# Performance work log

Hardware: AMD Instinct MI355X
Metric: run time of the kernel (lower is better)

The kernel has to match this reference:

```python
import jax, jax.numpy as jnp
import numpy as np

H, DH, BS = 12, 64, 64          # heads, head_dim, block_size
D, FF, L, EPS = 768, 3072, 12, 1e-12

def _ln(x, g, b):
    m = x.mean(-1, keepdims=True)
    v = ((x - m) ** 2).mean(-1, keepdims=True)
    return (x - m) * jax.lax.rsqrt(v + EPS) * g + b

def setup_inputs() -> dict:
    key = jax.random.key(0)
    ks = iter(jax.random.split(key, 40))
    B, S, IN, C = 2, 4096, 1280, 2
    nb = S // BS
    def p(shape, s=0.02):
        return jax.random.normal(next(ks), shape, jnp.float32) * s
    inp = dict(
        embeddings=jax.random.normal(next(ks), (B, S, IN), jnp.float32),
        attention_mask=jnp.ones((B, S), jnp.int32),
        Wp=p((IN, D)), bp=jnp.zeros((D,), jnp.float32),
        pos_emb=p((S, D)), tok_emb=p((D,)),
        lne_g=jnp.ones((D,), jnp.float32), lne_b=jnp.zeros((D,), jnp.float32),
        Wq=p((L, D, D)), bq=jnp.zeros((L, D), jnp.float32),
        Wk=p((L, D, D)), bk=jnp.zeros((L, D), jnp.float32),
        Wv=p((L, D, D)), bv=jnp.zeros((L, D), jnp.float32),
        Wo=p((L, D, D)), bo=jnp.zeros((L, D), jnp.float32),
        l1g=jnp.ones((L, D), jnp.float32), l1b=jnp.zeros((L, D), jnp.float32),
        W1=p((L, D, FF)), b1=jnp.zeros((L, FF), jnp.float32),
        W2=p((L, FF, D)), b2=jnp.zeros((L, D), jnp.float32),
        l2g=jnp.ones((L, D), jnp.float32), l2b=jnp.zeros((L, D), jnp.float32),
        Wc=p((D, C)), bc=jnp.zeros((C,), jnp.float32),
    )
    # BigBird pattern: each interior query block -> 2 global + 3 window + 3 random key blocks.
    # Random blocks are drawn once (deterministic) like HF's data-independent rand mask.
    rng = np.random.default_rng(0)
    idx, val = [], []
    for i in range(1, nb - 1):
        blocks = [0, nb - 1, i - 1, i, i + 1]
        v = [True, True, i - 1 != 0, True, i + 1 != nb - 1]  # dedupe window/global overlap
        forbid = set(blocks)
        allowed = [x for x in range(nb) if x not in forbid]
        r = rng.choice(allowed, size=3, replace=False).tolist()
        idx.append(blocks + r)
        val.append(v + [True, True, True])
    inp["blk_idx"] = jnp.asarray(np.array(idx, np.int32))    # [nb-2, 8]
    inp["blk_valid"] = jnp.asarray(np.array(val, bool))       # [nb-2, 8]
    return inp

def reference(embeddings, attention_mask, Wp, bp, pos_emb, tok_emb, lne_g, lne_b,
              Wq, bq, Wk, bk, Wv, bv, Wo, bo, l1g, l1b, W1, b1, W2, b2, l2g, l2b,
              Wc, bc, blk_idx, blk_valid):
    B, S, _ = embeddings.shape
    nb = S // BS
    na = blk_idx.shape[1]
    x = embeddings @ Wp + bp + pos_emb + tok_emb
    x = _ln(x, lne_g, lne_b)
    am = attention_mask.astype(jnp.float32)                       # [B,S]
    full_bias = ((am - 1.0) * 1e9)[:, None, None, None, :]        # [B,1,1,1,S]
    amb = am.reshape(B, nb, BS)
    am_g = amb[:, blk_idx].reshape(B, nb - 2, na * BS)            # gathered key mask
    vmask = jnp.repeat(blk_valid, BS, axis=-1)                    # [nb-2, na*BS]
    gb = jnp.where((am_g > 0) & vmask[None], 0.0, -1e9)[:, None, :, None, :]
    scale = 1.0 / np.sqrt(DH).astype(np.float32)

    def layer(x, p):
        wq, bq_, wk, bk_, wv, bv_, wo, bo_, g1, b1_, w1, bi1, w2, bi2, g2, b2_ = p
        q = (x @ wq + bq_).reshape(B, S, H, DH).transpose(0, 2, 1, 3)
        k = (x @ wk + bk_).reshape(B, S, H, DH).transpose(0, 2, 1, 3)
        v = (x @ wv + bv_).reshape(B, S, H, DH).transpose(0, 2, 1, 3)
        qb = q.reshape(B, H, nb, BS, DH)
        kb = k.reshape(B, H, nb, BS, DH)
        vb = v.reshape(B, H, nb, BS, DH)
        # interior query blocks: gather sparse key blocks (global+window+random)
        q_int = qb[:, :, 1:-1]                                     # [B,H,nb-2,BS,DH]
        k_g = kb[:, :, blk_idx].reshape(B, H, nb - 2, na * BS, DH)
        v_g = vb[:, :, blk_idx].reshape(B, H, nb - 2, na * BS, DH)
        s = jnp.einsum('bhiqd,bhikd->bhiqk', q_int, k_g) * scale + gb
        p_ = jax.nn.softmax(s, axis=-1)
        ctx_int = jnp.einsum('bhiqk,bhikd->bhiqd', p_, v_g)
        # first/last blocks are global: attend to all keys
        q_edge = jnp.stack([qb[:, :, 0], qb[:, :, -1]], axis=2)    # [B,H,2,BS,DH]
        se = jnp.einsum('bheqd,bhkd->bheqk', q_edge, k) * scale + full_bias
        pe = jax.nn.softmax(se, axis=-1)
        ctx_e = jnp.einsum('bheqk,bhkd->bheqd', pe, v)
        ctx = jnp.concatenate([ctx_e[:, :, :1], ctx_int, ctx_e[:, :, 1:]], axis=2)
        ctx = ctx.reshape(B, H, S, DH).transpose(0, 2, 1, 3).reshape(B, S, D)
        x = _ln(x + ctx @ wo + bo_, g1, b1_)
        h = jax.nn.gelu(x @ w1 + bi1, approximate=False) @ w2 + bi2
        x = _ln(x + h, g2, b2_)
        return x, None

    x, _ = jax.lax.scan(layer, x, (Wq, bq, Wk, bk, Wv, bv, Wo, bo,
                                   l1g, l1b, W1, b1, W2, b2, l2g, l2b))
    return x[:, 0, :] @ Wc + bc
```

## Files before the change

### kernel.cpp

```cpp
#include <hip/hip_runtime.h>
#include <hip/hip_bf16.h>
#include <math.h>

using bf16 = __hip_bfloat16;
typedef short bf16x8 __attribute__((ext_vector_type(8)));
typedef float f32x4 __attribute__((ext_vector_type(4)));
typedef unsigned short u16x4 __attribute__((ext_vector_type(4)));
typedef unsigned short u16x8 __attribute__((ext_vector_type(8)));
typedef short bf16x4v __attribute__((ext_vector_type(4)));

#define DEV __device__ __forceinline__

constexpr int BATCH = 2, SEQ = 4096, INPD = 1280, DM = 768, FFD = 3072;
constexpr int NL = 12, NH = 12, DHD = 64, NBLK = 64, NCLS = 2;
constexpr int MR = BATCH * SEQ;
constexpr int QKVN = 3 * DM;
constexpr int NJOBS = 62 + 16;
constexpr int PARTF = 64 * 64 + 128;

DEV void gload_lds16(const void* g, void* l) {
  __builtin_amdgcn_global_load_lds(
      (const __attribute__((address_space(1))) unsigned int*)g,
      (__attribute__((address_space(3))) unsigned int*)l, 16, 0, 0);
}

DEV f32x4 mfma16(bf16x8 a, bf16x8 b, f32x4 c) {
  return __builtin_amdgcn_mfma_f32_16x16x32_bf16(a, b, c, 0, 0, 0);
}

DEV float b2f(unsigned short u) { return __uint_as_float((unsigned)u << 16); }
DEV unsigned short f2b(float x) {
  bf16 h = __float2bfloat16(x);
  return *(unsigned short*)&h;
}

DEV int xcd_swizzle(int orig, int nwg) {
  int q = nwg >> 3, r = nwg & 7;
  int xcd = orig & 7, pos_ = orig >> 3;
  return (xcd < r ? xcd * (q + 1) : r * (q + 1) + (xcd - r) * q) + pos_;
}

__global__ void k_f32_to_bf16(const float* __restrict__ in, bf16* __restrict__ out, int n) {
  int i = (blockIdx.x * blockDim.x + threadIdx.x) * 8;
  int stride = gridDim.x * blockDim.x * 8;
  for (; i < n; i += stride) {
    float4 a = *(const float4*)(in + i);
    float4 b = *(const float4*)(in + i + 4);
    bf16 t8[8];
    t8[0] = __float2bfloat16(a.x); t8[1] = __float2bfloat16(a.y);
    t8[2] = __float2bfloat16(a.z); t8[3] = __float2bfloat16(a.w);
    t8[4] = __float2bfloat16(b.x); t8[5] = __float2bfloat16(b.y);
    t8[6] = __float2bfloat16(b.z); t8[7] = __float2bfloat16(b.w);
    *(bf16x8*)(out + i) = *(bf16x8*)t8;
  }
}

DEV void tr32_tile(const float* __restrict__ src, bf16* __restrict__ dst,
                   int K, int N, int tile, float t[32][33], int tid) {
  int nt = N >> 5;
  int tk = tile / nt, tn = tile - tk * nt;
  {
    int k = tid >> 3, c4 = (tid & 7) << 2;
    float4 v = *(const float4*)(src + (size_t)(tk * 32 + k) * N + tn * 32 + c4);
    t[k][c4 + 0] = v.x; t[k][c4 + 1] = v.y; t[k][c4 + 2] = v.z; t[k][c4 + 3] = v.w;
  }
  __syncthreads();
  {
    int n = tid >> 3, kc = (tid & 7) << 2;
    bf16 o4[4];
    o4[0] = __float2bfloat16(t[kc + 0][n]);
    o4[1] = __float2bfloat16(t[kc + 1][n]);
    o4[2] = __float2bfloat16(t[kc + 2][n]);
    o4[3] = __float2bfloat16(t[kc + 3][n]);
    *(bf16x4v*)(dst + (size_t)(tn * 32 + n) * K + tk * 32 + kc) = *(bf16x4v*)o4;
  }
}

__global__ __launch_bounds__(256) void k_transpose_one(const float* __restrict__ src,
                                                       bf16* __restrict__ dst, int K, int N) {
  __shared__ float t[32][33];
  tr32_tile(src, dst, K, N, blockIdx.x, t, threadIdx.x);
}

__global__ __launch_bounds__(256) void k_transpose_layer(
    const float* __restrict__ Wq, const float* __restrict__ Wk,
    const float* __restrict__ Wv, const float* __restrict__ Wo,
    const float* __restrict__ W1, const float* __restrict__ W2,
    bf16* __restrict__ wqkvT, bf16* __restrict__ woT,
    bf16* __restrict__ w1T, bf16* __restrict__ w2T, int l) {
  __shared__ float t[32][33];
  int id = blockIdx.x;
  const float* src; bf16* dst; int K, N;
  if (id < 1728) {
    int m = id / 576; id -= m * 576;
    src = (m == 0 ? Wq : m == 1 ? Wk : Wv) + (size_t)l * DM * DM;
    dst = wqkvT + (size_t)m * DM * DM; K = DM; N = DM;
  } else if (id < 2304) {
    id -= 1728; src = Wo + (size_t)l * DM * DM; dst = woT; K = DM; N = DM;
  } else if (id < 4608) {
    id -= 2304; src = W1 + (size_t)l * DM * FFD; dst = w1T; K = DM; N = FFD;
  } else {
    id -= 4608; src = W2 + (size_t)l * FFD * DM; dst = w2T; K = FFD; N = DM;
  }
  tr32_tile(src, dst, K, N, id, t, threadIdx.x);
}

template <int EPI>
__global__ __launch_bounds__(256) void k_gemm(
    const bf16* __restrict__ A, const bf16* __restrict__ BT, int N, int K,
    const float* __restrict__ b0, const float* __restrict__ pos, const float* __restrict__ tok,
    bf16* __restrict__ Cb) {
  __shared__ __align__(16) bf16 lA[2][128 * 32];
  __shared__ __align__(16) bf16 lB[2][128 * 32];
  const int tid = threadIdx.x;
  const int gx = gridDim.x;
  const int tile = xcd_swizzle(blockIdx.y * gx + blockIdx.x, gx * gridDim.y);
  const int bx = tile % gx, by = tile / gx;
  const int bm = by * 128, bn = bx * 128;
  const int lane = tid & 63, wid = tid >> 6;
  const int wm = (wid >> 1) * 64, wn = (wid & 1) * 64;
  const int lr = lane & 15, lks = lane >> 4;
  const bf16* Abase = A + (size_t)bm * K;
  const bf16* Bbase = BT + (size_t)bn * K;

  auto stage = [&](int buf, int t) {
    int k0 = t << 5;
#pragma unroll
    for (int ss = 0; ss < 2; ++ss) {
      int seg = tid + ss * 256;
      int row = seg >> 2, slot = seg & 3;
      int kseg = slot ^ ((row >> 1) & 3);
      gload_lds16(Abase + (size_t)row * K + k0 + kseg * 8, &lA[buf][seg * 8]);
      gload_lds16(Bbase + (size_t)row * K + k0 + kseg * 8, &lB[buf][seg * 8]);
    }
  };

  f32x4 acc[4][4] = {};
  const int nt = K >> 5;
  stage(0, 0);
  __syncthreads();
  for (int t = 0; t < nt; ++t) {
    const int buf = t & 1;
    if (t + 1 < nt) stage(buf ^ 1, t + 1);
    bf16x8 af[4], bfr[4];
#pragma unroll
    for (int m = 0; m < 4; ++m) {
      int rr = wm + m * 16 + lr;
      af[m] = *(const bf16x8*)(&lA[buf][rr * 32 + ((lks ^ ((rr >> 1) & 3)) << 3)]);
    }
#pragma unroll
    for (int n = 0; n < 4; ++n) {
      int rr = wn + n * 16 + lr;
      bfr[n] = *(const bf16x8*)(&lB[buf][rr * 32 + ((lks ^ ((rr >> 1) & 3)) << 3)]);
    }
#pragma unroll
    for (int m = 0; m < 4; ++m)
#pragma unroll
      for (int n = 0; n < 4; ++n)
        acc[m][n] = mfma16(af[m], bfr[n], acc[m][n]);
    __syncthreads();
  }
  const int gq = lane >> 4;
#pragma unroll
  for (int m = 0; m < 4; ++m) {
#pragma unroll
    for (int n = 0; n < 4; ++n) {
      int gcol = bn + wn + n * 16 + lr;
      f32x4 v = acc[m][n];
#pragma unroll
      for (int rr = 0; rr < 4; ++rr) {
        int grow = bm + wm + m * 16 + gq * 4 + rr;
        float x = v[rr];
        if constexpr (EPI == 2) {
          x += b0[gcol];
        } else {
          x += b0[gcol] + pos[(size_t)(grow & (SEQ - 1)) * N + gcol] + tok[gcol];
        }
        Cb[(size_t)grow * N + gcol] = __float2bfloat16(x);
      }
    }
  }
}

template <int EPI>
__global__ __launch_bounds__(512) void k_gemm_big(
    const bf16* __restrict__ A, const bf16* __restrict__ BT, int N, int K,
    const float* __restrict__ b0, const float* __restrict__ b1, const float* __restrict__ b2,
    bf16* __restrict__ Cb) {
  __shared__ __align__(16) bf16 lA[2][256 * 32];
  __shared__ __align__(16) bf16 lB[2][128 * 32];
  const int tid = threadIdx.x;
  const int gx = gridDim.x;
  const int tile = xcd_swizzle(blockIdx.y * gx + blockIdx.x, gx * gridDim.y);
  const int bx = tile % gx, by = tile / gx;
  const int bm = by * 256, bn = bx * 128;
  const int lane = tid & 63, wid = tid >> 6;
  const int wm = (wid >> 1) * 64, wn = (wid & 1) * 64;
  const int lr = lane & 15, lks = lane >> 4;
  const bf16* Abase = A + (size_t)bm * K;
  const bf16* Bbase = BT + (size_t)bn * K;

  auto stage = [&](int buf, int t) {
    int k0 = t << 5;
#pragma unroll
    for (int ss = 0; ss < 2; ++ss) {
      int seg = tid + ss * 512;
      int row = seg >> 2, slot = seg & 3;
      int kseg = slot ^ ((row >> 1) & 3);
      gload_lds16(Abase + (size_t)row * K + k0 + kseg * 8, &lA[buf][seg * 8]);
    }
    {
      int row = tid >> 2, slot = tid & 3;
      int kseg = slot ^ ((row >> 1) & 3);
      gload_lds16(Bbase + (size_t)row * K + k0 + kseg * 8, &lB[buf][tid * 8]);
    }
  };

  f32x4 acc[4][4] = {};
  const int nt = K >> 5;
  stage(0, 0);
  __syncthreads();
  for (int t = 0; t < nt; ++t) {
    const int buf = t & 1;
    if (t + 1 < nt) stage(buf ^ 1, t + 1);
    bf16x8 af[4], bfr[4];
#pragma unroll
    for (int m = 0; m < 4; ++m) {
      int rr = wm + m * 16 + lr;
      af[m] = *(const bf16x8*)(&lA[buf][rr * 32 + ((lks ^ ((rr >> 1) & 3)) << 3)]);
    }
#pragma unroll
    for (int n = 0; n < 4; ++n) {
      int rr = wn + n * 16 + lr;
      bfr[n] = *(const bf16x8*)(&lB[buf][rr * 32 + ((lks ^ ((rr >> 1) & 3)) << 3)]);
    }
#pragma unroll
    for (int m = 0; m < 4; ++m)
#pragma unroll
      for (int n = 0; n < 4; ++n)
        acc[m][n] = mfma16(af[m], bfr[n], acc[m][n]);
    __syncthreads();
  }
  const int gq = lane >> 4;
#pragma unroll
  for (int m = 0; m < 4; ++m) {
#pragma unroll
    for (int n = 0; n < 4; ++n) {
      int gcol = bn + wn + n * 16 + lr;
      f32x4 v = acc[m][n];
#pragma unroll
      for (int rr = 0; rr < 4; ++rr) {
        int grow = bm + wm + m * 16 + gq * 4 + rr;
        float x = v[rr];
        if constexpr (EPI == 0) {
          int c = gcol; const float* bb = b0;
          if (c >= 2 * DM) { bb = b2; c -= 2 * DM; }
          else if (c >= DM) { bb = b1; c -= DM; }
          x += bb[c];
        } else {
          x += b0[gcol];
          x = 0.5f * x * (1.0f + erff(x * 0.70710678118654752f));
        }
        Cb[(size_t)grow * N + gcol] = __float2bfloat16(x);
      }
    }
  }
}

template <bool HASRES>
__global__ __launch_bounds__(256) void k_ln_res(
    const bf16* __restrict__ gout, const bf16* res,
    const float* __restrict__ g, const float* __restrict__ b,
    bf16* out) {
  const int wv = threadIdx.x >> 6, lane = threadIdx.x & 63;
  const int row = blockIdx.x * 4 + wv;
  const unsigned short* gp = (const unsigned short*)gout + (size_t)row * DM;
  const unsigned short* rp = (const unsigned short*)res + (size_t)row * DM;
  float v[12];
  float s = 0.f, s2 = 0.f;
#pragma unroll
  for (int i = 0; i < 3; ++i) {
    const int c = i * 256 + lane * 4;
    u16x4 a4 = *(const u16x4*)(gp + c);
    u16x4 r4;
    if constexpr (HASRES) r4 = *(const u16x4*)(rp + c);
#pragma unroll
    for (int k2 = 0; k2 < 4; ++k2) {
      float x = b2f(a4[k2]);
      if constexpr (HASRES) x += b2f(r4[k2]);
      v[i * 4 + k2] = x;
      s += x; s2 += x * x;
    }
  }
#pragma unroll
  for (int off = 1; off < 64; off <<= 1) {
    s += __shfl_xor(s, off);
    s2 += __shfl_xor(s2, off);
  }
  const float mean = s * (1.0f / DM);
  const float var = s2 * (1.0f / DM) - mean * mean;
  const float rs = rsqrtf(var + 1e-12f);
  unsigned short* op = (unsigned short*)out + (size_t)row * DM;
#pragma unroll
  for (int i = 0; i < 3; ++i) {
    const int c = i * 256 + lane * 4;
    float4 g4 = *(const float4*)(g + c);
    float4 b4 = *(const float4*)(b + c);
    u16x4 o4;
    o4[0] = f2b((v[i * 4 + 0] - mean) * rs * g4.x + b4.x);
    o4[1] = f2b((v[i * 4 + 1] - mean) * rs * g4.y + b4.y);
    o4[2] = f2b((v[i * 4 + 2] - mean) * rs * g4.z + b4.z);
    o4[3] = f2b((v[i * 4 + 3] - mean) * rs * g4.w + b4.w);
    *(u16x4*)(op + c) = o4;
  }
}

__global__ __launch_bounds__(256) void k_vt(const bf16* __restrict__ qkv, bf16* __restrict__ vt) {
  __shared__ unsigned short t[64][72];
  const int bh = blockIdx.y, t0 = blockIdx.x * 64;
  const int b = bh / NH, h = bh - b * NH;
  const int tid = threadIdx.x;
  const int rr = tid >> 2, cs = (tid & 3) * 16;
  const unsigned short* src = (const unsigned short*)qkv +
      (size_t)(b * SEQ + t0 + rr) * QKVN + 2 * DM + h * DHD + cs;
  u16x8 v0 = *(const u16x8*)(src);
  u16x8 v1 = *(const u16x8*)(src + 8);
#pragma unroll
  for (int i = 0; i < 8; ++i) { t[cs + i][rr] = v0[i]; t[cs + 8 + i][rr] = v1[i]; }
  __syncthreads();
  unsigned short* dst = (unsigned short*)vt + (size_t)(bh * DHD + rr) * SEQ + t0 + cs;
  u16x8 o0, o1;
#pragma unroll
  for (int i = 0; i < 8; ++i) { o0[i] = t[rr][cs + i]; o1[i] = t[rr][cs + 8 + i]; }
  *(u16x8*)(dst) = o0;
  *(u16x8*)(dst + 8) = o1;
}

__global__ __launch_bounds__(256) void k_attn(
    const bf16* __restrict__ qkv, const bf16* __restrict__ vt,
    const int* __restrict__ blk_idx,
    bf16* __restrict__ ctx, float* __restrict__ epart) {
  __shared__ __align__(16) bf16 sQ[64 * 64];
  __shared__ __align__(16) bf16 sK[2][64 * 64];
  __shared__ __align__(16) bf16 sV[2][64 * 64];
  __shared__ __align__(16) bf16 sP[4][16 * 64];
  const int job = blockIdx.x;
  const int b = job / (NH * NJOBS);
  const int rem = job - b * NH * NJOBS;
  const int h = rem / NJOBS;
  const int j = rem - h * NJOBS;
  const int tid = threadIdx.x, lane = tid & 63, w = tid >> 6;
  const int lr = lane & 15, lks = lane >> 4;

  const bool interior = (j < 62);
  int qblk, e = 0, split = 0;
  if (interior) qblk = j + 1;
  else { int tt = j - 62; e = tt >> 3; split = tt & 7; qblk = e ? NBLK - 1 : 0; }
  const int qt0 = qblk * 64;

  const int skip_pos = interior ? (j == 0 ? 2 : (j == 61 ? 4 : 8)) : 8;
  const int nkb = (skip_pos < 8) ? 7 : 8;
  auto kbi_of = [&](int i) {
    int kb = i + (i >= skip_pos ? 1 : 0);
    return interior ? blk_idx[j * 8 + kb] : split * 8 + kb;
  };

  const bf16* kbase0 = qkv + (size_t)b * SEQ * QKVN + DM + h * DHD;
  const bf16* vbase0 = vt + (size_t)((b * NH + h) * DHD) * SEQ;
  auto stageKV = [&](int buf, int kbi) {
    const int kt0 = kbi * 64;
#pragma unroll
    for (int ss = 0; ss < 2; ++ss) {
      int seg = tid + ss * 256;
      int row = seg >> 3, slot = seg & 7;
      int kseg = slot ^ (row & 7);
      gload_lds16(kbase0 + (size_t)(kt0 + row) * QKVN + kseg * 8, &sK[buf][seg * 8]);
      gload_lds16(vbase0 + (size_t)row * SEQ + kt0 + kseg * 8, &sV[buf][seg * 8]);
    }
  };

  {
    const bf16* qbase = qkv + (size_t)(b * SEQ + qt0) * QKVN + h * DHD;
#pragma unroll
    for (int ss = 0; ss < 2; ++ss) {
      int seg = tid + ss * 256;
      int row = seg >> 3, slot = seg & 7;
      int kseg = slot ^ (row & 7);
      gload_lds16(qbase + (size_t)row * QKVN + kseg * 8, sQ + seg * 8);
    }
  }
  stageKV(0, kbi_of(0));
  __syncthreads();
  bf16x8 aq[2];
#pragma unroll
  for (int kk = 0; kk < 2; ++kk) {
    int rq = w * 16 + lr;
    int slot = (kk * 4 + lks) ^ (rq & 7);
    aq[kk] = *(const bf16x8*)(sQ + rq * 64 + slot * 8);
  }

  float m_r[4], l_r[4];
  f32x4 o[4] = {};
#pragma unroll
  for (int r = 0; r < 4; ++r) { m_r[r] = -1e30f; l_r[r] = 0.f; }

  for (int i = 0; i < nkb; ++i) {
    const int buf = i & 1;
    if (i + 1 < nkb) stageKV(buf ^ 1, kbi_of(i + 1));
    f32x4 sfr[4];
#pragma unroll
    for (int n = 0; n < 4; ++n) {
      f32x4 z = {};
#pragma unroll
      for (int kk = 0; kk < 2; ++kk) {
        int rk = n * 16 + lr;
        int slot = (kk * 4 + lks) ^ (rk & 7);
        bf16x8 kf = *(const bf16x8*)(&sK[buf][rk * 64 + slot * 8]);
        z = mfma16(aq[kk], kf, z);
      }
      sfr[n] = z;
    }
#pragma unroll
    for (int n = 0; n < 4; ++n)
#pragma unroll
      for (int r = 0; r < 4; ++r) sfr[n][r] *= 0.125f;
    float alpha[4];
#pragma unroll
    for (int r = 0; r < 4; ++r) {
      float tmx = fmaxf(fmaxf(sfr[0][r], sfr[1][r]), fmaxf(sfr[2][r], sfr[3][r]));
#pragma unroll
      for (int off = 1; off < 16; off <<= 1) tmx = fmaxf(tmx, __shfl_xor(tmx, off));
      float mnew = fmaxf(m_r[r], tmx);
      alpha[r] = __expf(m_r[r] - mnew);
      m_r[r] = mnew;
    }
#pragma unroll
    for (int r = 0; r < 4; ++r) {
      float su = 0.f;
#pragma unroll
      for (int n = 0; n < 4; ++n) {
        float p = __expf(sfr[n][r] - m_r[r]);
        sfr[n][r] = p;
        su += p;
      }
#pragma unroll
      for (int off = 1; off < 16; off <<= 1) su += __shfl_xor(su, off);
      l_r[r] = l_r[r] * alpha[r] + su;
    }
#pragma unroll
    for (int n = 0; n < 4; ++n) {
#pragma unroll
      for (int r = 0; r < 4; ++r) {
        int prow = lks * 4 + r;
        int col = n * 16 + lr;
        int eo = prow * 64 + ((((col >> 3) ^ (prow & 7)) << 3) | (col & 7));
        sP[w][eo] = __float2bfloat16(sfr[n][r]);
      }
    }
#pragma unroll
    for (int n = 0; n < 4; ++n)
#pragma unroll
      for (int r = 0; r < 4; ++r) o[n][r] *= alpha[r];
    asm volatile("s_waitcnt lgkmcnt(0)" ::: "memory");
    __builtin_amdgcn_sched_barrier(0);
    bf16x8 pa[2];
#pragma unroll
    for (int kk = 0; kk < 2; ++kk) {
      int slot = (kk * 4 + lks) ^ (lr & 7);
      pa[kk] = *(const bf16x8*)(sP[w] + lr * 64 + slot * 8);
    }
#pragma unroll
    for (int n = 0; n < 4; ++n) {
#pragma unroll
      for (int kk = 0; kk < 2; ++kk) {
        int rv = n * 16 + lr;
        int slot = (kk * 4 + lks) ^ (rv & 7);
        bf16x8 vf = *(const bf16x8*)(&sV[buf][rv * 64 + slot * 8]);
        o[n] = mfma16(pa[kk], vf, o[n]);
      }
    }
    __syncthreads();
  }
  if (interior) {
#pragma unroll
    for (int r = 0; r < 4; ++r) {
      float inv = 1.0f / l_r[r];
      int tok = qt0 + w * 16 + lks * 4 + r;
#pragma unroll
      for (int n = 0; n < 4; ++n) {
        int col = h * DHD + n * 16 + lr;
        ctx[(size_t)(b * SEQ + tok) * DM + col] = __float2bfloat16(o[n][r] * inv);
      }
    }
  } else {
    float* base = epart + (size_t)((((b * NH + h) * 2 + e) * 8) + split) * PARTF;
#pragma unroll
    for (int r = 0; r < 4; ++r) {
      int qrow = w * 16 + lks * 4 + r;
#pragma unroll
      for (int n = 0; n < 4; ++n)
        base[qrow * 64 + n * 16 + lr] = o[n][r];
      if (lr == 0) { base[4096 + qrow] = m_r[r]; base[4096 + 64 + qrow] = l_r[r]; }
    }
  }
}

__global__ __launch_bounds__(256) void k_combine(const float* __restrict__ epart,
                                                 bf16* __restrict__ ctx) {
  const int bid = blockIdx.x;
  const int b = bid / (NH * 2);
  const int rem = bid - b * NH * 2;
  const int h = rem >> 1, e = rem & 1;
  const int tid = threadIdx.x;
  const int row = tid >> 2, cq = tid & 3;
  const float* base0 = epart + (size_t)(((b * NH + h) * 2 + e) * 8) * PARTF;
  float ms[8], ls[8], M = -1e30f;
#pragma unroll
  for (int s = 0; s < 8; ++s) {
    const float* bp = base0 + (size_t)s * PARTF;
    ms[s] = bp[4096 + row];
    ls[s] = bp[4096 + 64 + row];
    M = fmaxf(M, ms[s]);
  }
  float Lt = 0.f, accv[16];
#pragma unroll
  for (int i = 0; i < 16; ++i) accv[i] = 0.f;
#pragma unroll
  for (int s = 0; s < 8; ++s) {
    float wgt = __expf(ms[s] - M);
    Lt += ls[s] * wgt;
    const float* op = base0 + (size_t)s * PARTF + row * 64 + cq * 16;
#pragma unroll
    for (int i = 0; i < 16; ++i) accv[i] += op[i] * wgt;
  }
  float inv = 1.0f / Lt;
  int qblk = e ? NBLK - 1 : 0;
  int tok = qblk * 64 + row;
  bf16* cp = ctx + (size_t)(b * SEQ + tok) * DM + h * DHD + cq * 16;
#pragma unroll
  for (int i = 0; i < 16; ++i) cp[i] = __float2bfloat16(accv[i] * inv);
}

__global__ void k_classifier(const bf16* __restrict__ xb, const float* __restrict__ Wc,
                             const float* __restrict__ bc, float* __restrict__ out) {
  const int tid = threadIdx.x, lane = tid & 63, wv = tid >> 6;
  const int b = wv >> 1, c = wv & 1;
  float s = 0.f;
  for (int d = lane; d < DM; d += 64)
    s += __bfloat162float(xb[(size_t)(b * SEQ) * DM + d]) * Wc[d * NCLS + c];
#pragma unroll
  for (int off = 32; off > 0; off >>= 1) s += __shfl_down(s, off);
  if (lane == 0) out[b * NCLS + c] = s + bc[c];
}

extern "C" void kernel_launch(void* const* d_in, const int* in_sizes, int n_in,
                              void* d_out, int out_size, void* d_ws, size_t ws_size,
                              hipStream_t stream) {
  const float* embeddings = (const float*)d_in[0];
  const float* Wp  = (const float*)d_in[2];
  const float* bp  = (const float*)d_in[3];
  const float* pos = (const float*)d_in[4];
  const float* tokv = (const float*)d_in[5];
  const float* lng = (const float*)d_in[6];
  const float* lnb = (const float*)d_in[7];
  const float* Wq  = (const float*)d_in[8];
  const float* bq  = (const float*)d_in[9];
  const float* Wk  = (const float*)d_in[10];
  const float* bk  = (const float*)d_in[11];
  const float* Wv  = (const float*)d_in[12];
  const float* bv  = (const float*)d_in[13];
  const float* Wo  = (const float*)d_in[14];
  const float* bo  = (const float*)d_in[15];
  const float* l1g = (const float*)d_in[16];
  const float* l1b = (const float*)d_in[17];
  const float* W1  = (const float*)d_in[18];
  const float* b1  = (const float*)d_in[19];
  const float* W2  = (const float*)d_in[20];
  const float* b2  = (const float*)d_in[21];
  const float* l2g = (const float*)d_in[22];
  const float* l2b = (const float*)d_in[23];
  const float* Wc  = (const float*)d_in[24];
  const float* bc  = (const float*)d_in[25];
  const int*  bidx = (const int*)d_in[26];
  (void)in_sizes; (void)n_in; (void)out_size; (void)ws_size;

  char* ws = (char*)d_ws;
  size_t off = 0;
  auto alloc = [&](size_t bytes) -> char* {
    char* p = ws + off;
    off += (bytes + 255) & ~(size_t)255;
    return p;
  };
  bf16*  embB  = (bf16*)alloc((size_t)MR * INPD * 2);
  bf16*  wpT   = (bf16*)alloc((size_t)DM * INPD * 2);
  bf16*  wqkvT = (bf16*)alloc((size_t)QKVN * DM * 2);
  bf16*  woT   = (bf16*)alloc((size_t)DM * DM * 2);
  bf16*  w1T   = (bf16*)alloc((size_t)FFD * DM * 2);
  bf16*  w2T   = (bf16*)alloc((size_t)DM * FFD * 2);
  bf16*  xb    = (bf16*)alloc((size_t)MR * DM * 2);
  bf16*  gout  = (bf16*)alloc((size_t)MR * DM * 2);
  bf16*  qkvB  = (bf16*)alloc((size_t)MR * QKVN * 2);
  bf16*  vtB   = (bf16*)alloc((size_t)BATCH * NH * DHD * SEQ * 2);
  bf16*  ctxB  = (bf16*)alloc((size_t)MR * DM * 2);
  bf16*  hB    = (bf16*)alloc((size_t)MR * FFD * 2);
  float* epart = (float*)alloc((size_t)BATCH * NH * 2 * 8 * PARTF * 4);

  k_f32_to_bf16<<<2048, 256, 0, stream>>>(embeddings, embB, MR * INPD);
  k_transpose_one<<<(INPD / 32) * (DM / 32), 256, 0, stream>>>(Wp, wpT, INPD, DM);
  k_gemm<3><<<dim3(DM / 128, MR / 128), 256, 0, stream>>>(embB, wpT, DM, INPD,
      bp, pos, tokv, gout);
  k_ln_res<false><<<MR / 4, 256, 0, stream>>>(gout, gout, lng, lnb, xb);

  for (int l = 0; l < NL; ++l) {
    k_transpose_layer<<<6912, 256, 0, stream>>>(Wq, Wk, Wv, Wo, W1, W2,
        wqkvT, woT, w1T, w2T, l);
    k_gemm_big<0><<<dim3(QKVN / 128, MR / 256), 512, 0, stream>>>(xb, wqkvT, QKVN, DM,
        bq + (size_t)l * DM, bk + (size_t)l * DM, bv + (size_t)l * DM, qkvB);
    k_vt<<<dim3(SEQ / 64, BATCH * NH), 256, 0, stream>>>(qkvB, vtB);
    k_attn<<<BATCH * NH * NJOBS, 256, 0, stream>>>(qkvB, vtB, bidx, ctxB, epart);
    k_combine<<<BATCH * NH * 2, 256, 0, stream>>>(epart, ctxB);
    k_gemm<2><<<dim3(DM / 128, MR / 128), 256, 0, stream>>>(ctxB, woT, DM, DM,
        bo + (size_t)l * DM, nullptr, nullptr, gout);
    k_ln_res<true><<<MR / 4, 256, 0, stream>>>(gout, xb,
        l1g + (size_t)l * DM, l1b + (size_t)l * DM, xb);
    k_gemm_big<1><<<dim3(FFD / 128, MR / 256), 512, 0, stream>>>(xb, w1T, FFD, DM,
        b1 + (size_t)l * FFD, nullptr, nullptr, hB);
    k_gemm<2><<<dim3(DM / 128, MR / 128), 256, 0, stream>>>(hB, w2T, DM, FFD,
        b2 + (size_t)l * DM, nullptr, nullptr, gout);
    k_ln_res<true><<<MR / 4, 256, 0, stream>>>(gout, xb,
        l2g + (size_t)l * DM, l2b + (size_t)l * DM, xb);
  }
  k_classifier<<<1, 256, 0, stream>>>(xb, Wc, bc, (float*)d_out);
}
```

Baseline: 3.504 ms.

## Prune last layer to CLS rows and fuse V transpose into QKV GEMM

The output reads only token 0 of each batch, so the final layer now computes attention for the first global query block only. Its output projection, LayerNorms and FFN run as GEMVs on two rows. Separately, the QKV GEMM epilogue writes V straight into the transposed layout, which removes the k_vt kernel and its extra pass over memory. The pruning is a legitimate dead-code elimination, but the last layer's K/V are still computed in full, and the transposed V write is a strided 8-byte scatter.

```diff
diff --git a/kernel.cpp b/kernel.cpp
--- a/kernel.cpp
+++ b/kernel.cpp
@@ -186,7 +186,7 @@
 __global__ __launch_bounds__(512) void k_gemm_big(
     const bf16* __restrict__ A, const bf16* __restrict__ BT, int N, int K,
     const float* __restrict__ b0, const float* __restrict__ b1, const float* __restrict__ b2,
-    bf16* __restrict__ Cb) {
+    bf16* __restrict__ vt, bf16* __restrict__ Cb) {
   __shared__ __align__(16) bf16 lA[2][256 * 32];
   __shared__ __align__(16) bf16 lB[2][128 * 32];
   const int tid = threadIdx.x;
@@ -247,21 +247,33 @@
 #pragma unroll
     for (int n = 0; n < 4; ++n) {
       int gcol = bn + wn + n * 16 + lr;
+      int grow0 = bm + wm + m * 16 + gq * 4;
       f32x4 v = acc[m][n];
-#pragma unroll
-      for (int rr = 0; rr < 4; ++rr) {
-        int grow = bm + wm + m * 16 + gq * 4 + rr;
-        float x = v[rr];
-        if constexpr (EPI == 0) {
-          int c = gcol; const float* bb = b0;
-          if (c >= 2 * DM) { bb = b2; c -= 2 * DM; }
-          else if (c >= DM) { bb = b1; c -= DM; }
-          x += bb[c];
+      if constexpr (EPI == 0) {
+        if (gcol < 2 * DM) {
+          const float* bb = (gcol < DM) ? b0 : b1;
+          float bias = bb[(gcol < DM) ? gcol : gcol - DM];
+#pragma unroll
+          for (int rr = 0; rr < 4; ++rr)
+            Cb[(size_t)(grow0 + rr) * N + gcol] = __float2bfloat16(v[rr] + bias);
         } else {
-          x += b0[gcol];
+          int c = gcol - 2 * DM;
+          float bias = b2[c];
+          int h = c >> 6, d = c & 63;
+          int bq_ = grow0 >> 12, s = grow0 & (SEQ - 1);
+          bf16 o4[4];
+#pragma unroll
+          for (int rr = 0; rr < 4; ++rr) o4[rr] = __float2bfloat16(v[rr] + bias);
+          *(bf16x4v*)(vt + ((size_t)((bq_ * NH + h) * DHD + d)) * SEQ + s) = *(bf16x4v*)o4;
+        }
+      } else {
+        float bias = b0[gcol];
+#pragma unroll
+        for (int rr = 0; rr < 4; ++rr) {
+          float x = v[rr] + bias;
           x = 0.5f * x * (1.0f + erff(x * 0.70710678118654752f));
+          Cb[(size_t)(grow0 + rr) * N + gcol] = __float2bfloat16(x);
         }
-        Cb[(size_t)grow * N + gcol] = __float2bfloat16(x);
       }
     }
   }
@@ -315,40 +327,19 @@
   }
 }
 
-__global__ __launch_bounds__(256) void k_vt(const bf16* __restrict__ qkv, bf16* __restrict__ vt) {
-  __shared__ unsigned short t[64][72];
-  const int bh = blockIdx.y, t0 = blockIdx.x * 64;
-  const int b = bh / NH, h = bh - b * NH;
-  const int tid = threadIdx.x;
-  const int rr = tid >> 2, cs = (tid & 3) * 16;
-  const unsigned short* src = (const unsigned short*)qkv +
-      (size_t)(b * SEQ + t0 + rr) * QKVN + 2 * DM + h * DHD + cs;
-  u16x8 v0 = *(const u16x8*)(src);
-  u16x8 v1 = *(const u16x8*)(src + 8);
-#pragma unroll
-  for (int i = 0; i < 8; ++i) { t[cs + i][rr] = v0[i]; t[cs + 8 + i][rr] = v1[i]; }
-  __syncthreads();
-  unsigned short* dst = (unsigned short*)vt + (size_t)(bh * DHD + rr) * SEQ + t0 + cs;
-  u16x8 o0, o1;
-#pragma unroll
-  for (int i = 0; i < 8; ++i) { o0[i] = t[rr][cs + i]; o1[i] = t[rr][cs + 8 + i]; }
-  *(u16x8*)(dst) = o0;
-  *(u16x8*)(dst + 8) = o1;
-}
-
 __global__ __launch_bounds__(256) void k_attn(
     const bf16* __restrict__ qkv, const bf16* __restrict__ vt,
     const int* __restrict__ blk_idx,
-    bf16* __restrict__ ctx, float* __restrict__ epart) {
+    bf16* __restrict__ ctx, float* __restrict__ epart, int nj, int jbase) {
   __shared__ __align__(16) bf16 sQ[64 * 64];
   __shared__ __align__(16) bf16 sK[2][64 * 64];
   __shared__ __align__(16) bf16 sV[2][64 * 64];
   __shared__ __align__(16) bf16 sP[4][16 * 64];
   const int job = blockIdx.x;
-  const int b = job / (NH * NJOBS);
-  const int rem = job - b * NH * NJOBS;
-  const int h = rem / NJOBS;
-  const int j = rem - h * NJOBS;
+  const int b = job / (NH * nj);
+  const int rem = job - b * NH * nj;
+  const int h = rem / nj;
+  const int j = jbase + (rem - h * nj);
   const int tid = threadIdx.x, lane = tid & 63, w = tid >> 6;
   const int lr = lane & 15, lks = lane >> 4;
 
@@ -506,11 +497,11 @@
 }
 
 __global__ __launch_bounds__(256) void k_combine(const float* __restrict__ epart,
-                                                 bf16* __restrict__ ctx) {
+                                                 bf16* __restrict__ ctx, int ne) {
   const int bid = blockIdx.x;
-  const int b = bid / (NH * 2);
-  const int rem = bid - b * NH * 2;
-  const int h = rem >> 1, e = rem & 1;
+  const int b = bid / (NH * ne);
+  const int rem = bid - b * NH * ne;
+  const int h = rem / ne, e = rem - (rem / ne) * ne;
   const int tid = threadIdx.x;
   const int row = tid >> 2, cq = tid & 3;
   const float* base0 = epart + (size_t)(((b * NH + h) * 2 + e) * 8) * PARTF;
@@ -541,13 +532,85 @@
   for (int i = 0; i < 16; ++i) cp[i] = __float2bfloat16(accv[i] * inv);
 }
 
-__global__ void k_classifier(const bf16* __restrict__ xb, const float* __restrict__ Wc,
+template <int ACT>
+__global__ __launch_bounds__(256) void k_gemv(
+    const bf16* __restrict__ X, size_t xstride, int K,
+    const bf16* __restrict__ WT, const float* __restrict__ bias,
+    float* __restrict__ Yf, bf16* __restrict__ Yb, int N) {
+  const int r = blockIdx.y;
+  const int tid = threadIdx.x;
+  const int col = blockIdx.x * 64 + (tid >> 2);
+  const int t4 = tid & 3;
+  const bf16* xp = X + (size_t)r * xstride;
+  const bf16* wp = WT + (size_t)col * K;
+  float s = 0.f;
+  for (int k = t4 * 8; k < K; k += 32) {
+    bf16x8 xv = *(const bf16x8*)(xp + k);
+    bf16x8 wv = *(const bf16x8*)(wp + k);
+#pragma unroll
+    for (int i = 0; i < 8; ++i)
+      s += b2f((unsigned short)xv[i]) * b2f((unsigned short)wv[i]);
+  }
+  s += __shfl_xor(s, 1);
+  s += __shfl_xor(s, 2);
+  if (t4 == 0) {
+    float x = s + bias[col];
+    if constexpr (ACT == 1) {
+      x = 0.5f * x * (1.0f + erff(x * 0.70710678118654752f));
+      Yb[(size_t)r * N + col] = __float2bfloat16(x);
+    } else {
+      Yf[(size_t)r * N + col] = x;
+    }
+  }
+}
+
+__global__ __launch_bounds__(128) void k_ln2(
+    const float* __restrict__ g2, const bf16* __restrict__ res, size_t rstride,
+    const float* __restrict__ g, const float* __restrict__ b, bf16* __restrict__ out2) {
+  const int r = threadIdx.x >> 6, lane = threadIdx.x & 63;
+  const float* gp = g2 + r * DM;
+  const unsigned short* rp = (const unsigned short*)res + (size_t)r * rstride;
+  float v[12];
+  float s = 0.f, s2 = 0.f;
+#pragma unroll
+  for (int i = 0; i < 3; ++i) {
+    const int c = i * 256 + lane * 4;
+    float4 a4 = *(const float4*)(gp + c);
+    u16x4 r4 = *(const u16x4*)(rp + c);
+    float xs[4] = {a4.x + b2f(r4[0]), a4.y + b2f(r4[1]), a4.z + b2f(r4[2]), a4.w + b2f(r4[3])};
+#pragma unroll
+    for (int k2 = 0; k2 < 4; ++k2) { v[i * 4 + k2] = xs[k2]; s += xs[k2]; s2 += xs[k2] * xs[k2]; }
+  }
+#pragma unroll
+  for (int off = 1; off < 64; off <<= 1) {
+    s += __shfl_xor(s, off);
+    s2 += __shfl_xor(s2, off);
+  }
+  const float mean = s * (1.0f / DM);
+  const float var = s2 * (1.0f / DM) - mean * mean;
+  const float rs = rsqrtf(var + 1e-12f);
+  unsigned short* op = (unsigned short*)out2 + (size_t)r * DM;
+#pragma unroll
+  for (int i = 0; i < 3; ++i) {
+    const int c = i * 256 + lane * 4;
+    float4 g4 = *(const float4*)(g + c);
+    float4 b4 = *(const float4*)(b + c);
+    u16x4 o4;
+    o4[0] = f2b((v[i * 4 + 0] - mean) * rs * g4.x + b4.x);
+    o4[1] = f2b((v[i * 4 + 1] - mean) * rs * g4.y + b4.y);
+    o4[2] = f2b((v[i * 4 + 2] - mean) * rs * g4.z + b4.z);
+    o4[3] = f2b((v[i * 4 + 3] - mean) * rs * g4.w + b4.w);
+    *(u16x4*)(op + c) = o4;
+  }
+}
+
+__global__ void k_classifier(const bf16* __restrict__ x2, const float* __restrict__ Wc,
                              const float* __restrict__ bc, float* __restrict__ out) {
   const int tid = threadIdx.x, lane = tid & 63, wv = tid >> 6;
   const int b = wv >> 1, c = wv & 1;
   float s = 0.f;
   for (int d = lane; d < DM; d += 64)
-    s += __bfloat162float(xb[(size_t)(b * SEQ) * DM + d]) * Wc[d * NCLS + c];
+    s += b2f(((const unsigned short*)x2)[b * DM + d]) * Wc[d * NCLS + c];
 #pragma unroll
   for (int off = 32; off > 0; off >>= 1) s += __shfl_down(s, off);
   if (lane == 0) out[b * NCLS + c] = s + bc[c];
@@ -604,6 +667,9 @@
   bf16*  ctxB  = (bf16*)alloc((size_t)MR * DM * 2);
   bf16*  hB    = (bf16*)alloc((size_t)MR * FFD * 2);
   float* epart = (float*)alloc((size_t)BATCH * NH * 2 * 8 * PARTF * 4);
+  float* g2    = (float*)alloc(2 * DM * 4);
+  bf16*  xb2   = (bf16*)alloc(2 * DM * 2);
+  bf16*  h2    = (bf16*)alloc(2 * FFD * 2);
 
   k_f32_to_bf16<<<2048, 256, 0, stream>>>(embeddings, embB, MR * INPD);
   k_transpose_one<<<(INPD / 32) * (DM / 32), 256, 0, stream>>>(Wp, wpT, INPD, DM);
@@ -611,24 +677,43 @@
       bp, pos, tokv, gout);
   k_ln_res<false><<<MR / 4, 256, 0, stream>>>(gout, gout, lng, lnb, xb);
 
-  for (int l = 0; l < NL; ++l) {
+  for (int l = 0; l < NL - 1; ++l) {
     k_transpose_layer<<<6912, 256, 0, stream>>>(Wq, Wk, Wv, Wo, W1, W2,
         wqkvT, woT, w1T, w2T, l);
     k_gemm_big<0><<<dim3(QKVN / 128, MR / 256), 512, 0, stream>>>(xb, wqkvT, QKVN, DM,
-        bq + (size_t)l * DM, bk + (size_t)l * DM, bv + (size_t)l * DM, qkvB);
-    k_vt<<<dim3(SEQ / 64, BATCH * NH), 256, 0, stream>>>(qkvB, vtB);
-    k_attn<<<BATCH * NH * NJOBS, 256, 0, stream>>>(qkvB, vtB, bidx, ctxB, epart);
-    k_combine<<<BATCH * NH * 2, 256, 0, stream>>>(epart, ctxB);
+        bq + (size_t)l * DM, bk + (size_t)l * DM, bv + (size_t)l * DM, vtB, qkvB);
+    k_attn<<<BATCH * NH * NJOBS, 256, 0, stream>>>(qkvB, vtB, bidx, ctxB, epart, NJOBS, 0);
+    k_combine<<<BATCH * NH * 2, 256, 0, stream>>>(epart, ctxB, 2);
     k_gemm<2><<<dim3(DM / 128, MR / 128), 256, 0, stream>>>(ctxB, woT, DM, DM,
         bo + (size_t)l * DM, nullptr, nullptr, gout);
     k_ln_res<true><<<MR / 4, 256, 0, stream>>>(gout, xb,
         l1g + (size_t)l * DM, l1b + (size_t)l * DM, xb);
     k_gemm_big<1><<<dim3(FFD / 128, MR / 256), 512, 0, stream>>>(xb, w1T, FFD, DM,
-        b1 + (size_t)l * FFD, nullptr, nullptr, hB);
+        b1 + (size_t)l * FFD, nullptr, nullptr, nullptr, hB);
     k_gemm<2><<<dim3(DM / 128, MR / 128), 256, 0, stream>>>(hB, w2T, DM, FFD,
         b2 + (size_t)l * DM, nullptr, nullptr, gout);
     k_ln_res<true><<<MR / 4, 256, 0, stream>>>(gout, xb,
         l2g + (size_t)l * DM, l2b + (size_t)l * DM, xb);
   }
-  k_classifier<<<1, 256, 0, stream>>>(xb, Wc, bc, (float*)d_out);
-}
+
+  {
+    const int l = NL - 1;
+    k_transpose_layer<<<6912, 256, 0, stream>>>(Wq, Wk, Wv, Wo, W1, W2,
+        wqkvT, woT, w1T, w2T, l);
+    k_gemm_big<0><<<dim3(QKVN / 128, MR / 256), 512, 0, stream>>>(xb, wqkvT, QKVN, DM,
+        bq + (size_t)l * DM, bk + (size_t)l * DM, bv + (size_t)l * DM, vtB, qkvB);
+    k_attn<<<BATCH * NH * 8, 256, 0, stream>>>(qkvB, vtB, bidx, ctxB, epart, 8, 62);
+    k_combine<<<BATCH * NH * 1, 256, 0, stream>>>(epart, ctxB, 1);
+    k_gemv<0><<<dim3(DM / 64, 2), 256, 0, stream>>>(ctxB, (size_t)SEQ * DM, DM,
+        woT, bo + (size_t)l * DM, g2, nullptr, DM);
+    k_ln2<<<1, 128, 0, stream>>>(g2, xb, (size_t)SEQ * DM,
+        l1g + (size_t)l * DM, l1b + (size_t)l * DM, xb2);
+    k_gemv<1><<<dim3(FFD / 64, 2), 256, 0, stream>>>(xb2, (size_t)DM, DM,
+        w1T, b1 + (size_t)l * FFD, nullptr, h2, FFD);
+    k_gemv<0><<<dim3(DM / 64, 2), 256, 0, stream>>>(h2, (size_t)FFD, FFD,
+        w2T, b2 + (size_t)l * DM, g2, nullptr, DM);
+    k_ln2<<<1, 128, 0, stream>>>(g2, xb2, (size_t)DM,
+        l2g + (size_t)l * DM, l2b + (size_t)l * DM, xb2);
+  }
+  k_classifier<<<1, 256, 0, stream>>>(xb2, Wc, bc, (float*)d_out);
+}
```

Measured after the change: 3.334 ms (median of 2 runs). -4.8%, faster.
